# Performance work log

Measured on AMD Instinct MI355X. Metric: run time of the kernel, lower is better.

The kernel has to match this reference:

```python
import jax, jax.numpy as jnp
import numpy as np

B, T, S, H, V = 4, 512, 1024, 768, 50257

def setup_inputs() -> dict:
    key = jax.random.key(0)
    k1, k2, k3, k4, k5, k6 = jax.random.split(key, 6)
    input_ids_to_copy = jax.random.randint(k1, (B, S), 0, V)
    cross_attentions = jax.random.uniform(k2, (B, T, S), dtype=jnp.float32)
    # normalize like attention weights
    cross_attentions = cross_attentions / jnp.sum(cross_attentions, axis=-1, keepdims=True)
    src_hidden_states = jax.random.normal(k3, (B, S, H), dtype=jnp.float32)
    tgt_hidden_states = jax.random.normal(k4, (B, T, H), dtype=jnp.float32)
    # p_gen_head = Linear(2H, 1) + Sigmoid
    W_pgen = jax.random.normal(k5, (2 * H, 1), dtype=jnp.float32) * (1.0 / np.sqrt(2 * H))
    b_pgen = jnp.zeros((1,), dtype=jnp.float32)
    return {
        "input_ids_to_copy": input_ids_to_copy,
        "cross_attentions": cross_attentions,
        "src_hidden_states": src_hidden_states,
        "tgt_hidden_states": tgt_hidden_states,
        "W_pgen": W_pgen,
        "b_pgen": b_pgen,
    }

def _copy_logits(attn_bts, ids_bs, vocab_size):
    # logits[b,t,v] = sum_s attn[b,t,s] * (ids[b,s] == v)
    # Efficient scatter-add over source positions instead of one-hot + matmul.
    def per_batch(attn_ts, ids_s):
        # attn_ts: [T,S], ids_s: [S] -> segment_sum over S -> [V,T] -> [T,V]
        return jax.ops.segment_sum(attn_ts.T, ids_s, num_segments=vocab_size).T
    return jax.vmap(per_batch)(attn_bts, ids_bs)

def reference(input_ids_to_copy, cross_attentions, src_hidden_states,
              tgt_hidden_states, W_pgen, b_pgen):
    # context_vectors: [B,T,H]
    context_vectors = jnp.einsum('bts,bsh->bth', cross_attentions, src_hidden_states)
    total_states = jnp.concatenate((context_vectors, tgt_hidden_states), axis=-1)  # [B,T,2H]
    p_gen = jax.nn.sigmoid(total_states @ W_pgen + b_pgen)  # [B,T,1]
    logits = _copy_logits(cross_attentions, input_ids_to_copy, V)  # [B,T,V]
    return (p_gen, logits)
```

## Files before the change

### kernel.cpp

```cpp
#include <hip/hip_runtime.h>
#include <hip/hip_bf16.h>
#include <math.h>

#define BB 4
#define TT 512
#define SS 1024
#define HH 768
#define VV 50257
#define NW 1571

__global__ __launch_bounds__(256) void proj_kernel(
    const float* __restrict__ src, const float* __restrict__ tgt,
    const float* __restrict__ W, const float* __restrict__ bptr,
    float* __restrict__ src_proj, float* __restrict__ tgt_proj)
{
    const int wave = threadIdx.x >> 6;
    const int lane = threadIdx.x & 63;
    const int row  = blockIdx.x * 4 + wave;

    const float* vec;
    const float* w;
    if (row < BB * SS) { vec = src + (size_t)row * HH;            w = W; }
    else               { vec = tgt + (size_t)(row - BB*SS) * HH;  w = W + HH; }
    const float4* v4 = (const float4*)vec;
    const float4* w4 = (const float4*)w;

    float acc = 0.f;
#pragma unroll
    for (int k = 0; k < 3; ++k) {
        float4 a = v4[k * 64 + lane];
        float4 b = w4[k * 64 + lane];
        acc += a.x * b.x + a.y * b.y + a.z * b.z + a.w * b.w;
    }
#pragma unroll
    for (int off = 32; off > 0; off >>= 1) acc += __shfl_down(acc, off);
    if (lane == 0) {
        if (row < BB * SS) src_proj[row] = acc;
        else               tgt_proj[row - BB * SS] = acc + bptr[0];
    }
}

__global__ __launch_bounds__(256) void batch_setup(
    const int* __restrict__ ids,
    unsigned* __restrict__ bm_g,
    unsigned* __restrict__ pre_g,
    unsigned short* __restrict__ rank_g)
{
    __shared__ unsigned bm[NW];
    __shared__ unsigned pre[NW];
    __shared__ unsigned scan[256];
    const int b = blockIdx.x, tid = threadIdx.x;

    for (int i = tid; i < NW; i += 256) bm[i] = 0u;
    __syncthreads();
    const int* idb = ids + b * SS;
    for (int s = tid; s < SS; s += 256) {
        const int v = idb[s];
        atomicOr(&bm[v >> 5], 1u << (v & 31));
    }
    __syncthreads();

    unsigned cnt[7];
    unsigned local = 0;
    const int w0 = tid * 7;
#pragma unroll
    for (int k = 0; k < 7; ++k) {
        const int w = w0 + k;
        cnt[k] = local;
        local += (w < NW) ? (unsigned)__popc(bm[w]) : 0u;
    }
    scan[tid] = local;
    __syncthreads();
    for (int off = 1; off < 256; off <<= 1) {
        const unsigned mine = scan[tid];
        const unsigned add  = (tid >= off) ? scan[tid - off] : 0u;
        __syncthreads();
        scan[tid] = mine + add;
        __syncthreads();
    }
    const unsigned excl = (tid > 0) ? scan[tid - 1] : 0u;
#pragma unroll
    for (int k = 0; k < 7; ++k) {
        const int w = w0 + k;
        if (w < NW) {
            const unsigned p = excl + cnt[k];
            pre[w] = p;
            pre_g[b * NW + w] = p;
            bm_g[b * NW + w]  = bm[w];
        }
    }
    __syncthreads();
    for (int s = tid; s < SS; s += 256) {
        const int v = idb[s];
        const unsigned w = (unsigned)v >> 5, bit = (unsigned)v & 31u;
        const unsigned r = pre[w] + (unsigned)__popc(bm[w] & ((1u << bit) - 1u));
        rank_g[b * SS + s] = (unsigned short)r;
    }
}

__device__ __forceinline__ float lut1(int v, const unsigned* bm,
                                      const unsigned* pre, const float* vals)
{
    const unsigned w = bm[v >> 5];
    const unsigned bit = (unsigned)v & 31u;
    if ((w >> bit) & 1u)
        return vals[pre[v >> 5] + (unsigned)__popc(w & ((1u << bit) - 1u))];
    return 0.f;
}

__global__ __launch_bounds__(256) void row_kernel(
    const float* __restrict__ attn,
    const float* __restrict__ src_proj,
    const float* __restrict__ tgt_proj,
    const unsigned* __restrict__ bm_g,
    const unsigned* __restrict__ pre_g,
    const unsigned short* __restrict__ rank_g,
    float* __restrict__ out)
{
    __shared__ unsigned bm[NW];
    __shared__ unsigned pre[NW];
    __shared__ unsigned short rnk[SS];
    __shared__ float vals[SS];
    __shared__ float wsum[4];

    const int row = blockIdx.x;
    const int b   = row >> 9;
    const int tid = threadIdx.x;

    for (int i = tid; i < NW; i += 256) { bm[i] = bm_g[b*NW+i]; pre[i] = pre_g[b*NW+i]; }
    for (int i = tid; i < SS; i += 256) rnk[i] = rank_g[b*SS+i];
    for (int i = tid; i < SS; i += 256) vals[i] = 0.f;
    __syncthreads();

    const float* arow = attn + (size_t)row * SS;
    const float* spb  = src_proj + b * SS;
    float acc = 0.f;
#pragma unroll
    for (int k = 0; k < SS / 256; ++k) {
        const int s = tid + k * 256;
        const float a = arow[s];
        atomicAdd(&vals[rnk[s]], a);
        acc += a * spb[s];
    }
#pragma unroll
    for (int off = 32; off > 0; off >>= 1) acc += __shfl_down(acc, off);
    if ((tid & 63) == 0) wsum[tid >> 6] = acc;
    __syncthreads();
    if (tid == 0) {
        const float x = wsum[0] + wsum[1] + wsum[2] + wsum[3] + tgt_proj[row];
        out[row] = 1.f / (1.f + expf(-x));
    }

    float* logits = out + (BB * TT) + (size_t)row * VV;
    const uintptr_t addr = (uintptr_t)logits;
    const int head = (int)(((16u - (unsigned)(addr & 15u)) & 15u) >> 2);
    if (tid < head) logits[tid] = lut1(tid, bm, pre, vals);

    const int n4 = (VV - head) >> 2;
    float4* p4 = (float4*)(logits + head);
    for (int i = tid; i < n4; i += 256) {
        const int v0 = head + (i << 2);
        float4 o = make_float4(0.f, 0.f, 0.f, 0.f);
        const unsigned w  = bm[v0 >> 5];
        const unsigned sh = (unsigned)v0 & 31u;
        unsigned nib;
        if (sh <= 28u) {
            nib = (w >> sh) & 0xFu;
        } else {
            const unsigned hi = bm[(v0 >> 5) + 1];
            nib = ((w >> sh) | (hi << (32u - sh))) & 0xFu;
        }
        if (nib) {
            o.x = lut1(v0,     bm, pre, vals);
            o.y = lut1(v0 + 1, bm, pre, vals);
            o.z = lut1(v0 + 2, bm, pre, vals);
            o.w = lut1(v0 + 3, bm, pre, vals);
        }
        p4[i] = o;
    }
    const int done = head + (n4 << 2);
    for (int v = done + tid; v < VV; v += 256)
        logits[v] = lut1(v, bm, pre, vals);
}

extern "C" void kernel_launch(void* const* d_in, const int* in_sizes, int n_in,
                              void* d_out, int out_size, void* d_ws, size_t ws_size,
                              hipStream_t stream) {
    const int*   ids  = (const int*)d_in[0];
    const float* attn = (const float*)d_in[1];
    const float* src  = (const float*)d_in[2];
    const float* tgt  = (const float*)d_in[3];
    const float* W    = (const float*)d_in[4];
    const float* bp   = (const float*)d_in[5];

    float* out = (float*)d_out;

    char* wsb = (char*)d_ws;
    float*          src_proj = (float*)wsb;
    float*          tgt_proj = src_proj + BB * SS;
    unsigned*       bm_g     = (unsigned*)(tgt_proj + BB * TT);
    unsigned*       pre_g    = bm_g + BB * NW;
    unsigned short* rank_g   = (unsigned short*)(pre_g + BB * NW);

    proj_kernel<<<(BB * SS + BB * TT) / 4, 256, 0, stream>>>(
        src, tgt, W, bp, src_proj, tgt_proj);
    batch_setup<<<BB, 256, 0, stream>>>(ids, bm_g, pre_g, rank_g);
    row_kernel<<<BB * TT, 256, 0, stream>>>(
        attn, src_proj, tgt_proj, bm_g, pre_g, rank_g, out);
}
```

Measured before the change: 466.6 us.

## Replace bitmap lookup with zero-fill plus sparse scatter of unique ids

Instead of a per-element bitmap/popcount lookup over the whole vocabulary row, the row kernel writes zeros in vocabulary chunks and then scatters the few nonzero values using a sorted unique-id list built in batch_setup. Per-block shared memory drops because the bitmap and prefix arrays are no longer loaded, and attention/rank loads are vectorized to float4/ushort4. Each chunk needs a block-wide barrier so zeros land before the sparse writes, which adds syncs and scattered 4-byte stores.

```diff
diff --git a/kernel.cpp b/kernel.cpp
--- a/kernel.cpp
+++ b/kernel.cpp
@@ -8,6 +8,8 @@
 #define HH 768
 #define VV 50257
 #define NW 1571
+#define CHUNK 2048
+#define NCH 25
 
 __global__ __launch_bounds__(256) void proj_kernel(
     const float* __restrict__ src, const float* __restrict__ tgt,
@@ -42,16 +44,17 @@
 
 __global__ __launch_bounds__(256) void batch_setup(
     const int* __restrict__ ids,
-    unsigned* __restrict__ bm_g,
-    unsigned* __restrict__ pre_g,
-    unsigned short* __restrict__ rank_g)
+    unsigned short* __restrict__ rank_g,
+    unsigned short* __restrict__ col_g)
 {
     __shared__ unsigned bm[NW];
     __shared__ unsigned pre[NW];
     __shared__ unsigned scan[256];
+    __shared__ unsigned short coll[SS];
     const int b = blockIdx.x, tid = threadIdx.x;
 
     for (int i = tid; i < NW; i += 256) bm[i] = 0u;
+    for (int i = tid; i < SS; i += 256) coll[i] = 0xFFFFu;
     __syncthreads();
     const int* idb = ids + b * SS;
     for (int s = tid; s < SS; s += 256) {
@@ -82,12 +85,7 @@
 #pragma unroll
     for (int k = 0; k < 7; ++k) {
         const int w = w0 + k;
-        if (w < NW) {
-            const unsigned p = excl + cnt[k];
-            pre[w] = p;
-            pre_g[b * NW + w] = p;
-            bm_g[b * NW + w]  = bm[w];
-        }
+        if (w < NW) pre[w] = excl + cnt[k];
     }
     __syncthreads();
     for (int s = tid; s < SS; s += 256) {
@@ -95,53 +93,54 @@
         const unsigned w = (unsigned)v >> 5, bit = (unsigned)v & 31u;
         const unsigned r = pre[w] + (unsigned)__popc(bm[w] & ((1u << bit) - 1u));
         rank_g[b * SS + s] = (unsigned short)r;
+        coll[r] = (unsigned short)v;
     }
-}
-
-__device__ __forceinline__ float lut1(int v, const unsigned* bm,
-                                      const unsigned* pre, const float* vals)
-{
-    const unsigned w = bm[v >> 5];
-    const unsigned bit = (unsigned)v & 31u;
-    if ((w >> bit) & 1u)
-        return vals[pre[v >> 5] + (unsigned)__popc(w & ((1u << bit) - 1u))];
-    return 0.f;
+    __syncthreads();
+    for (int i = tid; i < SS; i += 256) col_g[b * SS + i] = coll[i];
 }
 
 __global__ __launch_bounds__(256) void row_kernel(
     const float* __restrict__ attn,
     const float* __restrict__ src_proj,
     const float* __restrict__ tgt_proj,
-    const unsigned* __restrict__ bm_g,
-    const unsigned* __restrict__ pre_g,
     const unsigned short* __restrict__ rank_g,
+    const unsigned short* __restrict__ col_g,
     float* __restrict__ out)
 {
-    __shared__ unsigned bm[NW];
-    __shared__ unsigned pre[NW];
-    __shared__ unsigned short rnk[SS];
+    __shared__ unsigned short col[SS];
     __shared__ float vals[SS];
+    __shared__ int bnd[NCH + 1];
     __shared__ float wsum[4];
 
     const int row = blockIdx.x;
     const int b   = row >> 9;
     const int tid = threadIdx.x;
 
-    for (int i = tid; i < NW; i += 256) { bm[i] = bm_g[b*NW+i]; pre[i] = pre_g[b*NW+i]; }
-    for (int i = tid; i < SS; i += 256) rnk[i] = rank_g[b*SS+i];
-    for (int i = tid; i < SS; i += 256) vals[i] = 0.f;
+    for (int i = tid; i < SS; i += 256) { col[i] = col_g[b * SS + i]; vals[i] = 0.f; }
     __syncthreads();
 
-    const float* arow = attn + (size_t)row * SS;
-    const float* spb  = src_proj + b * SS;
-    float acc = 0.f;
-#pragma unroll
-    for (int k = 0; k < SS / 256; ++k) {
-        const int s = tid + k * 256;
-        const float a = arow[s];
-        atomicAdd(&vals[rnk[s]], a);
-        acc += a * spb[s];
+    const float4*  a4p = (const float4*)(attn + (size_t)row * SS);
+    const float4*  sp4 = (const float4*)(src_proj + b * SS);
+    const ushort4* r4p = (const ushort4*)(rank_g + b * SS);
+    const float4  a = a4p[tid];
+    const float4  p = sp4[tid];
+    const ushort4 r = r4p[tid];
+    atomicAdd(&vals[r.x], a.x);
+    atomicAdd(&vals[r.y], a.y);
+    atomicAdd(&vals[r.z], a.z);
+    atomicAdd(&vals[r.w], a.w);
+    float acc = a.x * p.x + a.y * p.y + a.z * p.z + a.w * p.w;
+
+    if (tid <= NCH) {
+        const unsigned short key = (unsigned short)(tid * CHUNK);
+        int lo = 0, hi = SS;
+        while (lo < hi) {
+            const int mid = (lo + hi) >> 1;
+            if (col[mid] < key) lo = mid + 1; else hi = mid;
+        }
+        bnd[tid] = lo;
     }
+
 #pragma unroll
     for (int off = 32; off > 0; off >>= 1) acc += __shfl_down(acc, off);
     if ((tid & 63) == 0) wsum[tid >> 6] = acc;
@@ -152,35 +151,21 @@
     }
 
     float* logits = out + (BB * TT) + (size_t)row * VV;
-    const uintptr_t addr = (uintptr_t)logits;
-    const int head = (int)(((16u - (unsigned)(addr & 15u)) & 15u) >> 2);
-    if (tid < head) logits[tid] = lut1(tid, bm, pre, vals);
+    const int head = (int)(((16u - (unsigned)((uintptr_t)logits & 15u)) & 15u) >> 2);
+    const float4 z4 = make_float4(0.f, 0.f, 0.f, 0.f);
 
-    const int n4 = (VV - head) >> 2;
-    float4* p4 = (float4*)(logits + head);
-    for (int i = tid; i < n4; i += 256) {
-        const int v0 = head + (i << 2);
-        float4 o = make_float4(0.f, 0.f, 0.f, 0.f);
-        const unsigned w  = bm[v0 >> 5];
-        const unsigned sh = (unsigned)v0 & 31u;
-        unsigned nib;
-        if (sh <= 28u) {
-            nib = (w >> sh) & 0xFu;
-        } else {
-            const unsigned hi = bm[(v0 >> 5) + 1];
-            nib = ((w >> sh) | (hi << (32u - sh))) & 0xFu;
-        }
-        if (nib) {
-            o.x = lut1(v0,     bm, pre, vals);
-            o.y = lut1(v0 + 1, bm, pre, vals);
-            o.z = lut1(v0 + 2, bm, pre, vals);
-            o.w = lut1(v0 + 3, bm, pre, vals);
-        }
-        p4[i] = o;
+    for (int c = 0; c < NCH; ++c) {
+        const int lo = c * CHUNK;
+        const int hi = (lo + CHUNK < VV) ? lo + CHUNK : VV;
+        if (tid < head) logits[lo + tid] = 0.f;
+        const int n4 = (hi - lo - head) >> 2;
+        float4* p4 = (float4*)(logits + lo + head);
+        for (int i = tid; i < n4; i += 256) p4[i] = z4;
+        for (int v = lo + head + (n4 << 2) + tid; v < hi; v += 256) logits[v] = 0.f;
+        __syncthreads();
+        for (int idx = bnd[c] + tid; idx < bnd[c + 1]; idx += 256)
+            logits[col[idx]] = vals[idx];
     }
-    const int done = head + (n4 << 2);
-    for (int v = done + tid; v < VV; v += 256)
-        logits[v] = lut1(v, bm, pre, vals);
 }
 
 extern "C" void kernel_launch(void* const* d_in, const int* in_sizes, int n_in,
@@ -195,16 +180,14 @@
 
     float* out = (float*)d_out;
 
-    char* wsb = (char*)d_ws;
-    float*          src_proj = (float*)wsb;
+    float*          src_proj = (float*)d_ws;
     float*          tgt_proj = src_proj + BB * SS;
-    unsigned*       bm_g     = (unsigned*)(tgt_proj + BB * TT);
-    unsigned*       pre_g    = bm_g + BB * NW;
-    unsigned short* rank_g   = (unsigned short*)(pre_g + BB * NW);
+    unsigned short* rank_g   = (unsigned short*)(tgt_proj + BB*TT);
+    unsigned short* col_g    = rank_g + BB * SS;
 
     proj_kernel<<<(BB * SS + BB * TT) / 4, 256, 0, stream>>>(
         src, tgt, W, bp, src_proj, tgt_proj);
-    batch_setup<<<BB, 256, 0, stream>>>(ids, bm_g, pre_g, rank_g);
+    batch_setup<<<BB, 256, 0, stream>>>(ids, rank_g, col_g);
     row_kernel<<<BB * TT, 256, 0, stream>>>(
-        attn, src_proj, tgt_proj, bm_g, pre_g, rank_g, out);
+        attn, src_proj, tgt_proj, rank_g, col_g, out);
 }
```

New measurement: 468.6 us. About the same (+0.4%).
